# Performance work log

Hardware: AMD Instinct MI355X
Metric: run time of the kernel (lower is better)

## Reference

```python
import jax, jax.numpy as jnp
import numpy as np

EPS = 1e-5  # equinox LayerNorm default eps

def setup_inputs() -> dict:
    key = jax.random.key(0)
    k1, k2, k3, k4, k5 = jax.random.split(key, 5)
    heads, d, dH, N = 16, 1024, 64, 2048
    # lecun-normal-ish scaling for fan_in=d
    s = 1.0 / np.sqrt(d)
    return {
        "x": jax.random.normal(k1, (d, N), dtype=jnp.float32),
        "WQ": jax.random.normal(k2, (heads, d, dH), dtype=jnp.float32) * s,
        "WK": jax.random.normal(k3, (heads, d, dH), dtype=jnp.float32) * s,
        "WV": jax.random.normal(k4, (heads, d, dH), dtype=jnp.float32) * s,
        "W0": jax.random.normal(k5, (d, d), dtype=jnp.float32) * s,
    }

def reference(x, WQ, WK, WV, W0):
    # x: [d, N]
    residual = x
    # equinox LayerNorm over full shape (d, N), no affine params
    mean = jnp.mean(x)
    var = jnp.var(x)
    xn = (x - mean) * jax.lax.rsqrt(var + EPS)
    # project: [h, d_model, dH] x [d_model, N] -> [h, dH, N]
    Q = jnp.einsum('hcd,ci->hdi', WQ, xn)
    K = jnp.einsum('hcd,ci->hdi', WK, xn)
    V = jnp.einsum('hcd,ci->hdi', WV, xn)
    dH = WK.shape[-1]
    dot = jnp.einsum('hdi,hdj->hij', Q, K)  # [h, N, N]
    alpha = jax.nn.softmax(dot / jnp.sqrt(jnp.asarray(dH, dot.dtype)), axis=-1)
    attn = jnp.einsum('hij,hdj->hdi', alpha, V)  # [h, dH, N]
    N = attn.shape[2]
    attn = attn.reshape(-1, N)  # [d, N]
    out = W0 @ attn
    return out + residual
```

## Files before the change

kernel.cpp:

```cpp
#include <hip/hip_runtime.h>
#include <math.h>

typedef unsigned short u16;
typedef _Float16 f16;
typedef __attribute__((ext_vector_type(8))) short bf16x8;
typedef __attribute__((ext_vector_type(8))) unsigned short u16x8;
typedef __attribute__((ext_vector_type(4))) float f32x4;
typedef __attribute__((ext_vector_type(4))) f16 f16x4;

#define D_MODEL 1024
#define SEQ_N   2048
#define HEADS   16
#define DHEAD   64
#define M3      3072
#define JSPLIT  4
#define JCHUNK  (SEQ_N / JSPLIT)

#define GLOBAL_AS __attribute__((address_space(1)))
#define LDS_AS    __attribute__((address_space(3)))
#define ASYNC16(gp, lp) __builtin_amdgcn_global_load_lds( \
    (const GLOBAL_AS unsigned int*)(gp), (LDS_AS unsigned int*)(lp), 16, 0, 0)

__device__ __forceinline__ u16 f2bf(float f) {
  union { float f; unsigned int u; } v; v.f = f;
  unsigned int r = v.u + 0x7fffu + ((v.u >> 16) & 1u);
  return (u16)(r >> 16);
}

__global__ __launch_bounds__(256) void ln_reduce1(const float* __restrict__ x,
                                                  double* __restrict__ part, int n4) {
  const float4* x4 = (const float4*)x;
  double s = 0.0, ss = 0.0;
  for (int idx = blockIdx.x * blockDim.x + threadIdx.x; idx < n4;
       idx += gridDim.x * blockDim.x) {
    float4 v = x4[idx];
    s  += (double)v.x + (double)v.y + (double)v.z + (double)v.w;
    ss += (double)v.x * v.x + (double)v.y * v.y + (double)v.z * v.z + (double)v.w * v.w;
  }
  __shared__ double ls[256], lss[256];
  int t = threadIdx.x;
  ls[t] = s; lss[t] = ss;
  __syncthreads();
  for (int off = 128; off > 0; off >>= 1) {
    if (t < off) { ls[t] += ls[t + off]; lss[t] += lss[t + off]; }
    __syncthreads();
  }
  if (t == 0) { part[2 * blockIdx.x] = ls[0]; part[2 * blockIdx.x + 1] = lss[0]; }
}

__global__ __launch_bounds__(256) void ln_norm_t(const float* __restrict__ x,
                                                 const double* __restrict__ part,
                                                 u16* __restrict__ xnt) {
  __shared__ float tile[64][65];
  __shared__ float sstat[2];
  int t = threadIdx.x;
  {
    double* ls = (double*)&tile[0][0];
    double* lss = ls + 256;
    ls[t]  = part[2 * t] + part[2 * (t + 256)];
    lss[t] = part[2 * t + 1] + part[2 * (t + 256) + 1];
    __syncthreads();
    for (int off = 128; off > 0; off >>= 1) {
      if (t < off) { ls[t] += ls[t + off]; lss[t] += lss[t + off]; }
      __syncthreads();
    }
    if (t == 0) {
      double inv = 1.0 / ((double)D_MODEL * (double)SEQ_N);
      double mean = ls[0] * inv;
      double var  = lss[0] * inv - mean * mean;
      sstat[0] = (float)mean;
      sstat[1] = (float)(1.0 / sqrt(var + 1e-5));
    }
    __syncthreads();
  }
  float mean = sstat[0], rstd = sstat[1];
  int ib = blockIdx.x * 64, cb = blockIdx.y * 64;
  __syncthreads();
#pragma unroll
  for (int r = 0; r < 4; ++r) {
    int c = (t >> 4) + r * 16;
    int i4 = (t & 15) * 4;
    float4 v = *(const float4*)(&x[(size_t)(cb + c) * SEQ_N + ib + i4]);
    tile[c][i4 + 0] = (v.x - mean) * rstd;
    tile[c][i4 + 1] = (v.y - mean) * rstd;
    tile[c][i4 + 2] = (v.z - mean) * rstd;
    tile[c][i4 + 3] = (v.w - mean) * rstd;
  }
  __syncthreads();
#pragma unroll
  for (int r = 0; r < 2; ++r) {
    int i = (t >> 3) + r * 32;
    int c8 = (t & 7) * 8;
    u16x8 o;
#pragma unroll
    for (int j = 0; j < 8; ++j) o[j] = f2bf(tile[c8 + j][i]);
    *(u16x8*)(&xnt[(size_t)(ib + i) * D_MODEL + cb + c8]) = o;
  }
}

__global__ __launch_bounds__(256) void pack_qkv(const float* __restrict__ WQ,
                                                const float* __restrict__ WK,
                                                const float* __restrict__ WV,
                                                u16* __restrict__ Wp) {
  __shared__ float tile[32][65];
  const float* W = (blockIdx.z == 0) ? WQ : ((blockIdx.z == 1) ? WK : WV);
  int h = blockIdx.y, cb = blockIdx.x * 32;
  int t = threadIdx.x;
  int dh = t & 63, cl = t >> 6;
  for (int r = 0; r < 8; ++r) {
    int c = cl + r * 4;
    tile[c][dh] = W[((size_t)h * D_MODEL + cb + c) * DHEAD + dh];
  }
  __syncthreads();
  int c2 = t & 31, d2 = t >> 5;
  for (int r = 0; r < 8; ++r) {
    int dd = d2 + r * 8;
    Wp[(size_t)((blockIdx.z * HEADS + h) * DHEAD + dd) * D_MODEL + cb + c2] =
        f2bf(tile[c2][dd]);
  }
}

__global__ __launch_bounds__(256) void pack_w0(const float* __restrict__ W0,
                                               u16* __restrict__ W0p, int n4) {
  int idx = blockIdx.x * blockDim.x + threadIdx.x;
  if (idx >= n4) return;
  float4 v = ((const float4*)W0)[idx];
  unsigned int lo = (unsigned int)f2bf(v.x) | ((unsigned int)f2bf(v.y) << 16);
  unsigned int hi = (unsigned int)f2bf(v.z) | ((unsigned int)f2bf(v.w) << 16);
  uint2 o; o.x = lo; o.y = hi;
  *(uint2*)(&W0p[(size_t)idx * 4]) = o;
}

__global__ __launch_bounds__(256) void gemm_qkv(const u16* __restrict__ A,
                                                const u16* __restrict__ Bt,
                                                u16* __restrict__ Qt,
                                                u16* __restrict__ Kt,
                                                f16* __restrict__ Vb) {
  __shared__ __align__(16) u16 Alds[128 * 32];
  __shared__ __align__(16) u16 Blds[64 * 32];
  int t = threadIdx.x;
  int lane = t & 63, w = t >> 6;
  int g = lane >> 4, l16 = lane & 15;
  int mb = blockIdx.y * 128, nb = blockIdx.x * 64;

  f32x4 acc[2][4];
#pragma unroll
  for (int i = 0; i < 2; ++i)
#pragma unroll
    for (int j = 0; j < 4; ++j) acc[i][j] = (f32x4){0.f, 0.f, 0.f, 0.f};

  int srow = t >> 2, scol = (t & 3) * 8;
  const u16* Ag0 = A + (size_t)(mb + srow) * D_MODEL + scol;
  const u16* Ag1 = A + (size_t)(mb + 64 + srow) * D_MODEL + scol;
  const u16* Bg  = Bt + (size_t)(nb + srow) * D_MODEL + scol;

  for (int kb = 0; kb < D_MODEL; kb += 32) {
    ASYNC16(Ag0 + kb, &Alds[t * 8]);
    ASYNC16(Ag1 + kb, &Alds[2048 + t * 8]);
    ASYNC16(Bg + kb, &Blds[t * 8]);
    __syncthreads();
    bf16x8 af[2], bf[4];
#pragma unroll
    for (int tm = 0; tm < 2; ++tm)
      af[tm] = *(const bf16x8*)(&Alds[(w * 32 + tm * 16 + l16) * 32 + g * 8]);
#pragma unroll
    for (int tn = 0; tn < 4; ++tn)
      bf[tn] = *(const bf16x8*)(&Blds[(tn * 16 + l16) * 32 + g * 8]);
#pragma unroll
    for (int tm = 0; tm < 2; ++tm)
#pragma unroll
      for (int tn = 0; tn < 4; ++tn)
        acc[tm][tn] = __builtin_amdgcn_mfma_f32_16x16x32_bf16(af[tm], bf[tn],
                                                              acc[tm][tn], 0, 0, 0);
    __syncthreads();
  }

#pragma unroll
  for (int tm = 0; tm < 2; ++tm) {
    int row0 = mb + w * 32 + tm * 16 + g * 4;
#pragma unroll
    for (int tn = 0; tn < 4; ++tn) {
      int col = nb + tn * 16 + l16;
      if (mb < 2 * D_MODEL) {
        u16* T = (mb < D_MODEL) ? Qt : Kt;
        int rbase = (mb < D_MODEL) ? row0 : row0 - D_MODEL;
        ushort4 o;
        o.x = f2bf(acc[tm][tn][0]); o.y = f2bf(acc[tm][tn][1]);
        o.z = f2bf(acc[tm][tn][2]); o.w = f2bf(acc[tm][tn][3]);
        *(ushort4*)(&T[(size_t)col * D_MODEL + rbase]) = o;
      } else {
        int rbase = row0 - 2 * D_MODEL;
#pragma unroll
        for (int r = 0; r < 4; ++r)
          Vb[(size_t)(rbase + r) * SEQ_N + col] = (f16)acc[tm][tn][r];
      }
    }
  }
}

__global__ __launch_bounds__(256) void gemm_bf16(const u16* __restrict__ A,
                                                 const u16* __restrict__ Bt,
                                                 float* __restrict__ C,
                                                 const float* __restrict__ res,
                                                 int M, int N, int K) {
  __shared__ __align__(16) u16 Alds[64 * 32];
  __shared__ __align__(16) u16 Blds[64 * 32];
  int t = threadIdx.x;
  int w = t >> 6, lane = t & 63;
  int g = lane >> 4, l16 = lane & 15;
  int mb = blockIdx.y * 64, nb = blockIdx.x * 64;
  f32x4 acc[4];
  for (int i = 0; i < 4; ++i) acc[i] = (f32x4){0.f, 0.f, 0.f, 0.f};
  int srow = t >> 2, scol = (t & 3) * 8;
  const u16* Ag = A + (size_t)(mb + srow) * K + scol;
  const u16* Bg = Bt + (size_t)(nb + srow) * K + scol;
  for (int kb = 0; kb < K; kb += 32) {
    ASYNC16(Ag + kb, &Alds[t * 8]);
    ASYNC16(Bg + kb, &Blds[t * 8]);
    __syncthreads();
    bf16x8 af = *(const bf16x8*)(&Alds[(w * 16 + l16) * 32 + g * 8]);
#pragma unroll
    for (int tn = 0; tn < 4; ++tn) {
      bf16x8 bf = *(const bf16x8*)(&Blds[(tn * 16 + l16) * 32 + g * 8]);
      acc[tn] = __builtin_amdgcn_mfma_f32_16x16x32_bf16(af, bf, acc[tn], 0, 0, 0);
    }
    __syncthreads();
  }
  int col0 = nb + l16;
  int row0 = mb + w * 16 + g * 4;
#pragma unroll
  for (int tn = 0; tn < 4; ++tn) {
    int col = col0 + tn * 16;
#pragma unroll
    for (int r = 0; r < 4; ++r) {
      int row = row0 + r;
      float v = acc[tn][r];
      if (res) v += res[(size_t)row * N + col];
      C[(size_t)row * N + col] = v;
    }
  }
}

__global__ __launch_bounds__(256, 8) void attn_mfma(const u16* __restrict__ Qt,
                                                    const u16* __restrict__ Kt,
                                                    const f16* __restrict__ Vb,
                                                    f16* __restrict__ Opart,
                                                    float* __restrict__ Lpart) {
  __shared__ __align__(16) u16 Klds[64][72];
  __shared__ __align__(16) f16 Vlds[64][72];
  int b = blockIdx.x;
  int xcd = b & 7, slot = b >> 3;
  int combo = xcd * 8 + (slot >> 5);
  int qt = slot & 31;
  int h = combo & 15;
  int sp = combo >> 4;
  int ib = qt * 64;
  int j0 = sp * JCHUNK;
  int t = threadIdx.x;
  int w = t >> 6, lane = t & 63;
  int g = lane >> 4, l16 = lane & 15;

  bf16x8 bq[2];
  {
    const u16* qb = Qt + (size_t)(ib + w * 16 + l16) * D_MODEL + h * DHEAD + g * 8;
    bq[0] = *(const bf16x8*)(qb);
    bq[1] = *(const bf16x8*)(qb + 32);
  }

  f32x4 acc_o[4];
#pragma unroll
  for (int i = 0; i < 4; ++i) acc_o[i] = (f32x4){0.f, 0.f, 0.f, 0.f};
  float lsum = 0.f;

  int srow = t >> 3, sch = (t & 7) * 8;
  for (int it = 0; it < JCHUNK / 64; ++it) {
    int jb = j0 + it * 64;
    uint4 kr0 = *(const uint4*)(&Kt[(size_t)(jb + srow) * D_MODEL + h * DHEAD + sch]);
    uint4 kr1 = *(const uint4*)(&Kt[(size_t)(jb + srow + 32) * D_MODEL + h * DHEAD + sch]);
    uint4 vr0 = *(const uint4*)(&Vb[(size_t)(h * DHEAD + srow) * SEQ_N + jb + sch]);
    uint4 vr1 = *(const uint4*)(&Vb[(size_t)(h * DHEAD + srow + 32) * SEQ_N + jb + sch]);
    *(uint4*)(&Klds[srow][sch]) = kr0;
    *(uint4*)(&Klds[srow + 32][sch]) = kr1;
    *(uint4*)(&Vlds[srow][sch]) = vr0;
    *(uint4*)(&Vlds[srow + 32][sch]) = vr1;
    __syncthreads();

    f32x4 s[4];
#pragma unroll
    for (int i = 0; i < 4; ++i) s[i] = (f32x4){0.f, 0.f, 0.f, 0.f};
#pragma unroll
    for (int kk = 0; kk < 2; ++kk)
#pragma unroll
      for (int tn = 0; tn < 4; ++tn) {
        bf16x8 ak = *(const bf16x8*)(&Klds[tn * 16 + l16][kk * 32 + g * 8]);
        s[tn] = __builtin_amdgcn_mfma_f32_16x16x32_bf16(ak, bq[kk], s[tn], 0, 0, 0);
      }
    f16x4 pf[4];
#pragma unroll
    for (int tn = 0; tn < 4; ++tn)
#pragma unroll
      for (int r = 0; r < 4; ++r) {
        float pv = exp2f(fmaf(s[tn][r], 0.18033688f, -5.7707801f));
        lsum += pv;
        pf[tn][r] = (f16)pv;
      }
#pragma unroll
    for (int tn = 0; tn < 4; ++tn)
#pragma unroll
      for (int td = 0; td < 4; ++td) {
        f16x4 bv = *(const f16x4*)(&Vlds[td * 16 + l16][tn * 16 + g * 4]);
        acc_o[td] =
            __builtin_amdgcn_mfma_f32_16x16x16f16(pf[tn], bv, acc_o[td], 0, 0, 0);
      }
    __syncthreads();
  }

  lsum += __shfl_xor(lsum, 16, 64);
  lsum += __shfl_xor(lsum, 32, 64);
  if (g == 0)
    Lpart[((size_t)sp * HEADS + h) * SEQ_N + ib + w * 16 + l16] = lsum;

#pragma unroll
  for (int td = 0; td < 4; ++td) {
    int dh = h * DHEAD + td * 16 + l16;
#pragma unroll
    for (int r = 0; r < 4; ++r) {
      int i = ib + w * 16 + g * 4 + r;
      Opart[((size_t)sp * SEQ_N + i) * D_MODEL + dh] = (f16)acc_o[td][r];
    }
  }
}

__global__ __launch_bounds__(256) void attn_combine(const f16* __restrict__ Opart,
                                                    const float* __restrict__ Lpart,
                                                    u16* __restrict__ attnt) {
  int i = blockIdx.x;
  int c = threadIdx.x * 4;
  int h = c >> 6;
  float l = 0.f;
#pragma unroll
  for (int s = 0; s < JSPLIT; ++s) l += Lpart[((size_t)s * HEADS + h) * SEQ_N + i];
  float o[4] = {0.f, 0.f, 0.f, 0.f};
#pragma unroll
  for (int s = 0; s < JSPLIT; ++s) {
    f16x4 v = *(const f16x4*)(&Opart[((size_t)s * SEQ_N + i) * D_MODEL + c]);
#pragma unroll
    for (int r = 0; r < 4; ++r) o[r] += (float)v[r];
  }
  float inv = 1.0f / l;
  ushort4 ob;
  ob.x = f2bf(o[0] * inv); ob.y = f2bf(o[1] * inv);
  ob.z = f2bf(o[2] * inv); ob.w = f2bf(o[3] * inv);
  *(ushort4*)(&attnt[(size_t)i * D_MODEL + c]) = ob;
}

extern "C" void kernel_launch(void* const* d_in, const int* in_sizes, int n_in,
                              void* d_out, int out_size, void* d_ws, size_t ws_size,
                              hipStream_t stream) {
  const float* x  = (const float*)d_in[0];
  const float* WQ = (const float*)d_in[1];
  const float* WK = (const float*)d_in[2];
  const float* WV = (const float*)d_in[3];
  const float* W0 = (const float*)d_in[4];
  float* out = (float*)d_out;

  char* ws = (char*)d_ws;
  size_t off = 0;
  double* part  = (double*)(ws + off); off += 8192;
  u16*    xnt   = (u16*)(ws + off); off += (size_t)SEQ_N * D_MODEL * 2;
  u16*    Wp    = (u16*)(ws + off); off += (size_t)M3 * D_MODEL * 2;
  u16*    W0p   = (u16*)(ws + off); off += (size_t)D_MODEL * D_MODEL * 2;
  u16*    Qt    = (u16*)(ws + off); off += (size_t)SEQ_N * D_MODEL * 2;
  u16*    Kt    = (u16*)(ws + off); off += (size_t)SEQ_N * D_MODEL * 2;
  f16*    Vb    = (f16*)(ws + off); off += (size_t)D_MODEL * SEQ_N * 2;
  u16*    attnt = (u16*)(ws + off); off += (size_t)SEQ_N * D_MODEL * 2;
  f16*    Opart = (f16*)(ws + off); off += (size_t)JSPLIT * SEQ_N * D_MODEL * 2;
  float*  Lpart = (float*)(ws + off); off += (size_t)JSPLIT * HEADS * SEQ_N * 4;

  ln_reduce1<<<512, 256, 0, stream>>>(x, part, (D_MODEL * SEQ_N) / 4);
  ln_norm_t<<<dim3(SEQ_N / 64, D_MODEL / 64), 256, 0, stream>>>(x, part, xnt);
  pack_qkv<<<dim3(D_MODEL / 32, HEADS, 3), 256, 0, stream>>>(WQ, WK, WV, Wp);
  pack_w0<<<(D_MODEL * D_MODEL / 4 + 255) / 256, 256, 0, stream>>>(W0, W0p,
                                                                   D_MODEL * D_MODEL / 4);
  gemm_qkv<<<dim3(SEQ_N / 64, M3 / 128), 256, 0, stream>>>(Wp, xnt, Qt, Kt, Vb);
  attn_mfma<<<2048, 256, 0, stream>>>(Qt, Kt, Vb, Opart, Lpart);
  attn_combine<<<SEQ_N, 256, 0, stream>>>(Opart, Lpart, attnt);
  gemm_bf16<<<dim3(SEQ_N / 64, D_MODEL / 64), 256, 0, stream>>>(W0p, attnt, out, x,
                                                                D_MODEL, SEQ_N, D_MODEL);
}
```

Baseline: 183.6 us.

## Stage GEMM and attention epilogues through LDS and remap blocks per XCD

The QKV GEMM epilogue now writes its tile into a shared-memory buffer that is unioned with the staging arrays, then emits coalesced 16-byte global stores instead of scattered 8-byte and 2-byte writes. The attention kernel's Opart output is staged through the V LDS buffer in the same way. Both GEMMs switch to a 1D grid with an XCD-aware tile mapping so blocks on the same XCD share A rows in L2. The cost is extra LDS traffic and barriers in the epilogue, plus a hard-coded assumption of 8 XCDs and M divisible by 512.

```diff
diff --git a/kernel.cpp b/kernel.cpp
--- a/kernel.cpp
+++ b/kernel.cpp
@@ -136,12 +136,20 @@
                                                 u16* __restrict__ Qt,
                                                 u16* __restrict__ Kt,
                                                 f16* __restrict__ Vb) {
-  __shared__ __align__(16) u16 Alds[128 * 32];
-  __shared__ __align__(16) u16 Blds[64 * 32];
+  union SM {
+    struct { u16 A[128 * 32]; u16 B[64 * 32]; } st;
+    u16 qk[64][130];
+    u16 v[128][66];
+  };
+  __shared__ __align__(16) SM sm;
   int t = threadIdx.x;
   int lane = t & 63, w = t >> 6;
   int g = lane >> 4, l16 = lane & 15;
-  int mb = blockIdx.y * 128, nb = blockIdx.x * 64;
+  int b = blockIdx.x;
+  int xcd = b & 7, s = b >> 3;
+  int mt = xcd * 3 + (s % 3);
+  int nt = s / 3;
+  int mb = mt * 128, nb = nt * 64;
 
   f32x4 acc[2][4];
 #pragma unroll
@@ -155,17 +163,17 @@
   const u16* Bg  = Bt + (size_t)(nb + srow) * D_MODEL + scol;
 
   for (int kb = 0; kb < D_MODEL; kb += 32) {
-    ASYNC16(Ag0 + kb, &Alds[t * 8]);
-    ASYNC16(Ag1 + kb, &Alds[2048 + t * 8]);
-    ASYNC16(Bg + kb, &Blds[t * 8]);
+    ASYNC16(Ag0 + kb, &sm.st.A[t * 8]);
+    ASYNC16(Ag1 + kb, &sm.st.A[2048 + t * 8]);
+    ASYNC16(Bg + kb, &sm.st.B[t * 8]);
     __syncthreads();
     bf16x8 af[2], bf[4];
 #pragma unroll
     for (int tm = 0; tm < 2; ++tm)
-      af[tm] = *(const bf16x8*)(&Alds[(w * 32 + tm * 16 + l16) * 32 + g * 8]);
+      af[tm] = *(const bf16x8*)(&sm.st.A[(w * 32 + tm * 16 + l16) * 32 + g * 8]);
 #pragma unroll
     for (int tn = 0; tn < 4; ++tn)
-      bf[tn] = *(const bf16x8*)(&Blds[(tn * 16 + l16) * 32 + g * 8]);
+      bf[tn] = *(const bf16x8*)(&sm.st.B[(tn * 16 + l16) * 32 + g * 8]);
 #pragma unroll
     for (int tm = 0; tm < 2; ++tm)
 #pragma unroll
@@ -175,25 +183,49 @@
     __syncthreads();
   }
 
-#pragma unroll
-  for (int tm = 0; tm < 2; ++tm) {
-    int row0 = mb + w * 32 + tm * 16 + g * 4;
-#pragma unroll
-    for (int tn = 0; tn < 4; ++tn) {
-      int col = nb + tn * 16 + l16;
-      if (mb < 2 * D_MODEL) {
-        u16* T = (mb < D_MODEL) ? Qt : Kt;
-        int rbase = (mb < D_MODEL) ? row0 : row0 - D_MODEL;
+  if (mb < 2 * D_MODEL) {
+#pragma unroll
+    for (int tm = 0; tm < 2; ++tm) {
+      int m0 = w * 32 + tm * 16 + g * 4;
+#pragma unroll
+      for (int tn = 0; tn < 4; ++tn) {
+        int nl = tn * 16 + l16;
         ushort4 o;
         o.x = f2bf(acc[tm][tn][0]); o.y = f2bf(acc[tm][tn][1]);
         o.z = f2bf(acc[tm][tn][2]); o.w = f2bf(acc[tm][tn][3]);
-        *(ushort4*)(&T[(size_t)col * D_MODEL + rbase]) = o;
-      } else {
-        int rbase = row0 - 2 * D_MODEL;
+        *(ushort4*)(&sm.qk[nl][m0]) = o;
+      }
+    }
+    __syncthreads();
+    u16* T = (mb < D_MODEL) ? Qt : Kt;
+    int mbase = (mb < D_MODEL) ? mb : mb - D_MODEL;
+#pragma unroll
+    for (int p = 0; p < 4; ++p) {
+      int row = p * 16 + (t >> 4);
+      int ch = (t & 15) * 8;
+      *(uint4*)(&T[(size_t)(nb + row) * D_MODEL + mbase + ch]) =
+          *(const uint4*)(&sm.qk[row][ch]);
+    }
+  } else {
+#pragma unroll
+    for (int tm = 0; tm < 2; ++tm) {
+      int m0 = w * 32 + tm * 16 + g * 4;
+#pragma unroll
+      for (int tn = 0; tn < 4; ++tn) {
+        int nl = tn * 16 + l16;
 #pragma unroll
         for (int r = 0; r < 4; ++r)
-          Vb[(size_t)(rbase + r) * SEQ_N + col] = (f16)acc[tm][tn][r];
+          ((f16*)&sm.v[m0 + r][0])[nl] = (f16)acc[tm][tn][r];
       }
+    }
+    __syncthreads();
+    int mbase = mb - 2 * D_MODEL;
+#pragma unroll
+    for (int p = 0; p < 4; ++p) {
+      int row = p * 32 + (t >> 3);
+      int ch = (t & 7) * 8;
+      *(uint4*)(&Vb[(size_t)(mbase + row) * SEQ_N + nb + ch]) =
+          *(const uint4*)(&sm.v[row][ch]);
     }
   }
 }
@@ -208,7 +240,12 @@
   int t = threadIdx.x;
   int w = t >> 6, lane = t & 63;
   int g = lane >> 4, l16 = lane & 15;
-  int mb = blockIdx.y * 64, nb = blockIdx.x * 64;
+  int b = blockIdx.x;
+  int xcd = b & 7, s = b >> 3;
+  int mpx = M / 512;
+  int mt = xcd * mpx + (s % mpx);
+  int nt = s / mpx;
+  int mb = mt * 64, nb = nt * 64;
   f32x4 acc[4];
   for (int i = 0; i < 4; ++i) acc[i] = (f32x4){0.f, 0.f, 0.f, 0.f};
   int srow = t >> 2, scol = (t & 3) * 8;
@@ -322,12 +359,18 @@
 
 #pragma unroll
   for (int td = 0; td < 4; ++td) {
-    int dh = h * DHEAD + td * 16 + l16;
-#pragma unroll
-    for (int r = 0; r < 4; ++r) {
-      int i = ib + w * 16 + g * 4 + r;
-      Opart[((size_t)sp * SEQ_N + i) * D_MODEL + dh] = (f16)acc_o[td][r];
-    }
+    int dhl = td * 16 + l16;
+#pragma unroll
+    for (int r = 0; r < 4; ++r)
+      Vlds[w * 16 + g * 4 + r][dhl] = (f16)acc_o[td][r];
+  }
+  __syncthreads();
+#pragma unroll
+  for (int p = 0; p < 2; ++p) {
+    int row = p * 32 + (t >> 3);
+    int ch = (t & 7) * 8;
+    *(uint4*)(&Opart[((size_t)sp * SEQ_N + ib + row) * D_MODEL + h * DHEAD + ch]) =
+        *(const uint4*)(&Vlds[row][ch]);
   }
 }
 
@@ -382,9 +425,9 @@
   pack_qkv<<<dim3(D_MODEL / 32, HEADS, 3), 256, 0, stream>>>(WQ, WK, WV, Wp);
   pack_w0<<<(D_MODEL * D_MODEL / 4 + 255) / 256, 256, 0, stream>>>(W0, W0p,
                                                                    D_MODEL * D_MODEL / 4);
-  gemm_qkv<<<dim3(SEQ_N / 64, M3 / 128), 256, 0, stream>>>(Wp, xnt, Qt, Kt, Vb);
+  gemm_qkv<<<(M3 / 128) * (SEQ_N / 64), 256, 0, stream>>>(Wp, xnt, Qt, Kt, Vb);
   attn_mfma<<<2048, 256, 0, stream>>>(Qt, Kt, Vb, Opart, Lpart);
   attn_combine<<<SEQ_N, 256, 0, stream>>>(Opart, Lpart, attnt);
-  gemm_bf16<<<dim3(SEQ_N / 64, D_MODEL / 64), 256, 0, stream>>>(W0p, attnt, out, x,
-                                                                D_MODEL, SEQ_N, D_MODEL);
-}
+  gemm_bf16<<<(D_MODEL / 64) * (SEQ_N / 64), 256, 0, stream>>>(W0p, attnt, out, x,
+                                                               D_MODEL, SEQ_N, D_MODEL);
+}
```

After: 183.4 us. About the same (-0.1%).
